# Kernel optimization log

Measured on AMD Instinct MI355X. Metric: run time of the kernel, lower is better.

The kernel has to match this reference:

```python
import jax, jax.numpy as jnp
import numpy as np

EMB = 1024
HID = 2048
NH = 16
NKV = 16
NE = 8
TOPK = 2
WIN = 2048
B = 2
L = 2048
HD = EMB // NH  # 64


def _layer_norm(x, g, b, eps=1e-5):
    m = jnp.mean(x, axis=-1, keepdims=True)
    v = jnp.mean((x - m) ** 2, axis=-1, keepdims=True)
    return (x - m) / jnp.sqrt(v + eps) * g + b


def setup_inputs() -> dict:
    key = jax.random.key(0)
    ks = jax.random.split(key, 12)
    w = lambda k, shape: (jax.random.normal(k, shape, jnp.float32) * 0.02)
    return {
        "x": jax.random.normal(ks[0], (B, L, EMB), jnp.float32),
        "position_idx": 0,
        "ln1_g": jnp.ones((EMB,), jnp.float32),
        "ln1_b": jnp.zeros((EMB,), jnp.float32),
        "ln2_g": jnp.ones((EMB,), jnp.float32),
        "ln2_b": jnp.zeros((EMB,), jnp.float32),
        "Wq": w(ks[1], (EMB, EMB)),
        "Wk": w(ks[2], (EMB, EMB)),
        "Wv": w(ks[3], (EMB, EMB)),
        "Wo": w(ks[4], (EMB, EMB)),
        "Wr": w(ks[5], (EMB, NE)),
        "W1": w(ks[6], (NE, EMB, HID)),
        "b1": jnp.zeros((NE, HID), jnp.float32),
        "W2": w(ks[7], (NE, HID, EMB)),
        "b2": jnp.zeros((NE, EMB), jnp.float32),
    }


def reference(x, position_idx, ln1_g, ln1_b, ln2_g, ln2_b, Wq, Wk, Wv, Wo, Wr, W1, b1, W2, b2):
    Bn, Ln, D = x.shape
    scale = 1.0 / (HD ** 0.5)

    # --- sliding-window attention (cache=None path) ---
    h = _layer_norm(x, ln1_g, ln1_b)
    q = (h @ Wq).reshape(Bn, Ln, NH, HD).transpose(0, 2, 1, 3)   # [B,H,L,hd]
    k = (h @ Wk).reshape(Bn, Ln, NKV, HD).transpose(0, 2, 1, 3)  # [B,KV,L,hd]
    v = (h @ Wv).reshape(Bn, Ln, NKV, HD).transpose(0, 2, 1, 3)
    k = k[:, :, -WIN:]
    v = v[:, :, -WIN:]
    qpk = NH // NKV
    if qpk > 1:
        k = jnp.repeat(k, qpk, axis=1)
        v = jnp.repeat(v, qpk, axis=1)
    scores = jnp.einsum('bhqd,bhkd->bhqk', q, k) * scale
    S = k.shape[2]
    i = jnp.arange(Ln)[:, None]
    j = jnp.arange(S)[None, :]
    mask = (j > i) | (j < i + position_idx - WIN)  # causal + sliding window
    scores = jnp.where(mask[None, None], -jnp.inf, scores)
    attn = jax.nn.softmax(scores, axis=-1)
    attn_out = jnp.einsum('bhqk,bhkd->bqhd', attn, v).reshape(Bn, Ln, D) @ Wo
    x = x + attn_out

    # --- top-k MoE ---
    h2 = _layer_norm(x, ln2_g, ln2_b)
    logits = h2 @ Wr                               # [B,L,E]
    top_v, top_i = jax.lax.top_k(logits, TOPK)     # [B,L,K]
    top_w = jax.nn.softmax(top_v, axis=-1)
    out = jnp.zeros_like(x)
    for e in range(NE):
        # combine weight for expert e per token (sums over top-k slots)
        we = jnp.sum(jnp.where(top_i == e, top_w, 0.0), axis=-1)  # [B,L]
        he = jax.nn.silu(h2 @ W1[e] + b1[e])
        out = out + we[..., None] * (he @ W2[e] + b2[e])
    return x + out
```

## Files before the change

kernel.cpp:

```cpp
#include <hip/hip_runtime.h>
#include <hip/hip_bf16.h>

typedef __hip_bfloat16 bf16;
typedef __attribute__((ext_vector_type(8))) short bf16x8;
typedef __attribute__((ext_vector_type(4))) float f32x4;

constexpr int kEMB = 1024;
constexpr int kHID = 2048;
constexpr int kNH  = 16;
constexpr int kNE  = 8;
constexpr int kL   = 2048;
constexpr int kHD  = 64;
constexpr int kT   = 4096;
constexpr int kSLOTS = kT * 2;
constexpr int kWIN = 2048;

__device__ __forceinline__ unsigned short f2bfbits(float f){
  bf16 h = __float2bfloat16(f);
  return __builtin_bit_cast(unsigned short, h);
}
__device__ __forceinline__ float bfbits2f(unsigned short u){
  unsigned int x = ((unsigned int)u) << 16;
  return __builtin_bit_cast(float, x);
}
__device__ __forceinline__ void gld_lds16(const void* g, void* s){
  __builtin_amdgcn_global_load_lds((const __attribute__((address_space(1))) void*)g,
                                   (__attribute__((address_space(3))) void*)s, 16, 0, 0);
}

__global__ __launch_bounds__(256) void tconv_k(const float* __restrict__ src, bf16* __restrict__ dst,
                                               int R, int C){
  __shared__ float tile[32][33];
  const int tx = threadIdx.x & 31, ty = threadIdx.x >> 5;
  const int bx = blockIdx.x * 32, by = blockIdx.y * 32;
  const size_t base = (size_t)blockIdx.z * R * C;
  #pragma unroll
  for (int i = 0; i < 32; i += 8)
    tile[ty + i][tx] = src[base + (size_t)(by + ty + i) * C + bx + tx];
  __syncthreads();
  #pragma unroll
  for (int i = 0; i < 32; i += 8)
    dst[base + (size_t)(bx + ty + i) * R + by + tx] = __float2bfloat16(tile[tx][ty + i]);
}

__global__ __launch_bounds__(256) void vtrans_k(const bf16* __restrict__ v, bf16* __restrict__ vt){
  __shared__ unsigned short tile[32][33];
  const int tx = threadIdx.x & 31, ty = threadIdx.x >> 5;
  const int l0 = blockIdx.x * 32, d0 = blockIdx.y * 32;
  const unsigned short* src = (const unsigned short*)v + (size_t)blockIdx.z * kL * kHD;
  unsigned short* dst = (unsigned short*)vt + (size_t)blockIdx.z * kHD * kL;
  #pragma unroll
  for (int i = 0; i < 32; i += 8)
    tile[ty + i][tx] = src[(size_t)(l0 + ty + i) * kHD + d0 + tx];
  __syncthreads();
  #pragma unroll
  for (int i = 0; i < 32; i += 8)
    dst[(size_t)(d0 + ty + i) * kL + l0 + tx] = tile[tx][ty + i];
}

__device__ __forceinline__ float block_sum(float v, float* red){
  #pragma unroll
  for (int x = 32; x > 0; x >>= 1) v += __shfl_xor(v, x, 64);
  const int lane = threadIdx.x & 63, w = threadIdx.x >> 6;
  if (lane == 0) red[w] = v;
  __syncthreads();
  float s = red[0] + red[1] + red[2] + red[3];
  __syncthreads();
  return s;
}

__global__ __launch_bounds__(256) void ln_k(
    const float* __restrict__ x, const float* __restrict__ g, const float* __restrict__ bta,
    bf16* __restrict__ h)
{
  __shared__ float red[4];
  const int row = blockIdx.x, tid = threadIdx.x;
  const float4 v = ((const float4*)(x + (size_t)row * kEMB))[tid];
  float s = block_sum(v.x + v.y + v.z + v.w, red);
  const float mean = s * (1.0f / kEMB);
  const float dx = v.x - mean, dy = v.y - mean, dz = v.z - mean, dw = v.w - mean;
  float ss = block_sum(dx*dx + dy*dy + dz*dz + dw*dw, red);
  const float rstd = rsqrtf(ss * (1.0f / kEMB) + 1e-5f);
  const float4 gg = ((const float4*)g)[tid];
  const float4 bb = ((const float4*)bta)[tid];
  ushort4 pk;
  pk.x = f2bfbits(dx * rstd * gg.x + bb.x);
  pk.y = f2bfbits(dy * rstd * gg.y + bb.y);
  pk.z = f2bfbits(dz * rstd * gg.z + bb.z);
  pk.w = f2bfbits(dw * rstd * gg.w + bb.w);
  *(ushort4*)((unsigned short*)h + (size_t)row * kEMB + tid * 4) = pk;
}

__global__ __launch_bounds__(256) void ln2_k(
    const float* __restrict__ x, const float* __restrict__ P,
    const float* __restrict__ g, const float* __restrict__ bta,
    float* __restrict__ out, bf16* __restrict__ h, const float* __restrict__ Wr,
    int* __restrict__ top_i, float* __restrict__ top_w)
{
  __shared__ float red[4];
  __shared__ float red8[4][8];
  const int row = blockIdx.x, tid = threadIdx.x;
  const float4 vx = ((const float4*)(x + (size_t)row * kEMB))[tid];
  const float4 p0 = ((const float4*)(P + (size_t)row * kEMB))[tid];
  const float4 p1 = ((const float4*)(P + (size_t)(kT + row) * kEMB))[tid];
  float4 v;
  v.x = vx.x + p0.x + p1.x; v.y = vx.y + p0.y + p1.y;
  v.z = vx.z + p0.z + p1.z; v.w = vx.w + p0.w + p1.w;
  ((float4*)(out + (size_t)row * kEMB))[tid] = v;
  float s = block_sum(v.x + v.y + v.z + v.w, red);
  const float mean = s * (1.0f / kEMB);
  const float dx = v.x - mean, dy = v.y - mean, dz = v.z - mean, dw = v.w - mean;
  float ss = block_sum(dx*dx + dy*dy + dz*dz + dw*dw, red);
  const float rstd = rsqrtf(ss * (1.0f / kEMB) + 1e-5f);
  const float4 gg = ((const float4*)g)[tid];
  const float4 bb = ((const float4*)bta)[tid];
  const float n0 = dx * rstd * gg.x + bb.x;
  const float n1 = dy * rstd * gg.y + bb.y;
  const float n2 = dz * rstd * gg.z + bb.z;
  const float n3 = dw * rstd * gg.w + bb.w;
  ushort4 pk;
  pk.x = f2bfbits(n0); pk.y = f2bfbits(n1); pk.z = f2bfbits(n2); pk.w = f2bfbits(n3);
  *(ushort4*)((unsigned short*)h + (size_t)row * kEMB + tid * 4) = pk;
  float part[8];
  #pragma unroll
  for (int e = 0; e < 8; e++) part[e] = 0.f;
  const float* wrp = Wr + (size_t)tid * 4 * kNE;
  const float nv[4] = {n0, n1, n2, n3};
  #pragma unroll
  for (int i = 0; i < 4; i++)
    #pragma unroll
    for (int e = 0; e < 8; e++) part[e] += nv[i] * wrp[i * kNE + e];
  #pragma unroll
  for (int xm = 32; xm > 0; xm >>= 1)
    #pragma unroll
    for (int e = 0; e < 8; e++) part[e] += __shfl_xor(part[e], xm, 64);
  const int lane = tid & 63, w = tid >> 6;
  if (lane == 0)
    #pragma unroll
    for (int e = 0; e < 8; e++) red8[w][e] = part[e];
  __syncthreads();
  if (tid == 0){
    float lg[8];
    #pragma unroll
    for (int e = 0; e < 8; e++) lg[e] = red8[0][e] + red8[1][e] + red8[2][e] + red8[3][e];
    int i0 = 0; float v0 = lg[0];
    #pragma unroll
    for (int e = 1; e < 8; e++) if (lg[e] > v0){ v0 = lg[e]; i0 = e; }
    int i1 = -1; float v1 = -3.4e38f;
    #pragma unroll
    for (int e = 0; e < 8; e++) if (e != i0 && lg[e] > v1){ v1 = lg[e]; i1 = e; }
    const float w0 = 1.0f / (1.0f + __expf(v1 - v0));
    top_i[row * 2] = i0; top_i[row * 2 + 1] = i1;
    top_w[row * 2] = w0; top_w[row * 2 + 1] = 1.0f - w0;
  }
}

template<int MODE>
__global__ __launch_bounds__(256) void gemm_k(
    const bf16* __restrict__ A, const bf16* __restrict__ BT, int K,
    float* __restrict__ fdst, bf16* __restrict__ bdst,
    const float* __restrict__ bias,
    const float* __restrict__ roww, const int* __restrict__ rowtok,
    const int* __restrict__ offs)
{
  __shared__ alignas(16) unsigned short As[2][128 * 64];
  __shared__ alignas(16) unsigned short Bs[2][128 * 64];
  const int tid = threadIdx.x, lane = tid & 63, w = tid >> 6;
  const int wr = w >> 1, wc = w & 1;
  int e = 0, rbase = 0, rend = 0, bx, by;
  if (MODE == 2){
    e = blockIdx.x & 7; const int s = blockIdx.x >> 3; by = s >> 4; bx = s & 15;
    rbase = offs[e]; rend = offs[e + 1];
    if (by * 128 >= rend - rbase) return;
  } else if (MODE == 3){
    e = blockIdx.x & 7; const int s = blockIdx.x >> 3; by = s >> 3; bx = s & 7;
    rbase = offs[e]; rend = offs[e + 1];
    if (by * 128 >= rend - rbase) return;
  } else {
    bx = blockIdx.x; by = blockIdx.y;
  }
  int kt0 = 0, nkt = K / 64;
  if (MODE == 1){ kt0 = blockIdx.z * (K / 2); nkt = K / 128; }
  const int m0 = by * 128, n0 = bx * 128;
  const bf16* Bp = BT;
  const float* biasp = bias;
  if (MODE == 2){ Bp += (size_t)e * kHID * kEMB; biasp += e * kHID; }
  if (MODE == 3){ Bp += (size_t)e * kEMB * kHID; biasp += e * kEMB; }
  f32x4 acc[4][4] = {};
  const int srow = lane >> 3;
  const int skk  = (lane & 7) * 8;

  size_t aoff[4];
  #pragma unroll
  for (int j = 0; j < 4; j++){
    const int r = w * 32 + j * 8 + srow;
    size_t row;
    if (MODE == 2){ int p = rbase + m0 + r; if (p >= rend) p = rbase; row = (size_t)rowtok[p]; }
    else if (MODE == 3){ int p = rbase + m0 + r; if (p >= rend) p = rbase; row = (size_t)p; }
    else row = (size_t)(m0 + r);
    aoff[j] = row * (size_t)K;
  }

  auto stage = [&](int t, int buf){
    const int kt = kt0 + t * 64;
    #pragma unroll
    for (int j = 0; j < 4; j++){
      const int rr = w * 32 + j * 8;
      gld_lds16(A + aoff[j] + kt + skk, &As[buf][rr * 64]);
      gld_lds16(Bp + (size_t)(n0 + rr + srow) * K + kt + skk, &Bs[buf][rr * 64]);
    }
  };

  stage(0, 0);
  __syncthreads();
  for (int t = 0; t < nkt; t++){
    const int cur = t & 1;
    if (t + 1 < nkt) stage(t + 1, cur ^ 1);
    #pragma unroll
    for (int ks = 0; ks < 2; ks++){
      bf16x8 af[4], bfm[4];
      #pragma unroll
      for (int i = 0; i < 4; i++){
        af[i]  = *(const bf16x8*)&As[cur][(wr * 64 + i * 16 + (lane & 15)) * 64 + ks * 32 + (lane >> 4) * 8];
        bfm[i] = *(const bf16x8*)&Bs[cur][(wc * 64 + i * 16 + (lane & 15)) * 64 + ks * 32 + (lane >> 4) * 8];
      }
      #pragma unroll
      for (int i = 0; i < 4; i++)
        #pragma unroll
        for (int j = 0; j < 4; j++)
          acc[i][j] = __builtin_amdgcn_mfma_f32_16x16x32_bf16(af[i], bfm[j], acc[i][j], 0, 0, 0);
    }
    __syncthreads();
  }

  #pragma unroll
  for (int i = 0; i < 4; i++){
    #pragma unroll
    for (int r = 0; r < 4; r++){
      const int gm = m0 + wr * 64 + i * 16 + (lane >> 4) * 4 + r;
      if (MODE == 1){
        float* pdst = fdst + (size_t)blockIdx.z * kT * kEMB;
        #pragma unroll
        for (int jn = 0; jn < 4; jn++){
          const int gn = n0 + wc * 64 + jn * 16 + (lane & 15);
          pdst[(size_t)gm * kEMB + gn] = acc[i][jn][r];
        }
      } else if (MODE == 2){
        const int p = rbase + gm;
        if (p < rend){
          #pragma unroll
          for (int jn = 0; jn < 4; jn++){
            const int gn = n0 + wc * 64 + jn * 16 + (lane & 15);
            const float vv = acc[i][jn][r] + biasp[gn];
            bdst[(size_t)p * kHID + gn] = __float2bfloat16(vv / (1.0f + __expf(-vv)));
          }
        }
      } else if (MODE == 3){
        const int p = rbase + gm;
        if (p < rend){
          const float wgt = roww[p];
          #pragma unroll
          for (int jn = 0; jn < 4; jn++){
            const int gn = n0 + wc * 64 + jn * 16 + (lane & 15);
            bdst[(size_t)p * kEMB + gn] = __float2bfloat16((acc[i][jn][r] + biasp[gn]) * wgt);
          }
        }
      } else {
        const int bidx = gm >> 11, l = gm & (kL - 1);
        #pragma unroll
        for (int jn = 0; jn < 4; jn++){
          const int gn = n0 + wc * 64 + jn * 16 + (lane & 15);
          const int sec = gn >> 10;
          const int nn = gn & 1023;
          const int hh = nn >> 6, d = nn & 63;
          const float val = acc[i][jn][r] * (sec == 0 ? 0.125f : 1.0f);
          bdst[(size_t)sec * kT * kEMB + (((size_t)bidx * kNH + hh) * kL + l) * kHD + d] =
              __float2bfloat16(val);
        }
      }
    }
  }
}

__global__ __launch_bounds__(256) void attn_k(
    const bf16* __restrict__ q, const bf16* __restrict__ k, const bf16* __restrict__ vt,
    bf16* __restrict__ o, const int* __restrict__ pos)
{
  const int bid = blockIdx.x;
  const int qt = 31 - (bid >> 5);
  const int bh = bid & 31;
  const int tid = threadIdx.x, lane = tid & 63, w = tid >> 6;
  const unsigned short* qp  = (const unsigned short*)q  + (size_t)bh * kL * kHD;
  const unsigned short* kp  = (const unsigned short*)k  + (size_t)bh * kL * kHD;
  const unsigned short* vtp = (const unsigned short*)vt + (size_t)bh * kHD * kL;
  __shared__ alignas(16) unsigned short Ks[2][64 * 64];
  __shared__ alignas(16) unsigned short Vt[2][64 * 64];
  __shared__ alignas(16) unsigned short pl[4 * 16 * 72];
  const int q0 = qt * 64 + w * 16;
  const int pos0 = pos[0];
  const int wlo = pos0 - kWIN;

  bf16x8 qf[2];
  {
    const int qrow = q0 + (lane & 15);
    #pragma unroll
    for (int ks = 0; ks < 2; ks++)
      qf[ks] = *(const bf16x8*)&qp[(size_t)qrow * kHD + ks * 32 + (lane >> 4) * 8];
  }
  float m_run[4], l_part[4];
  f32x4 oacc[4] = {};
  #pragma unroll
  for (int r = 0; r < 4; r++){ m_run[r] = -1e30f; l_part[r] = 0.f; }

  auto stage = [&](int kt, int buf){
    #pragma unroll
    for (int j = 0; j < 2; j++){
      const int r = w * 16 + j * 8 + (lane >> 3);
      const int c = (lane & 7) ^ (r & 7);
      gld_lds16(kp  + (size_t)(kt * 64 + r) * 64 + c * 8, &Ks[buf][(w * 16 + j * 8) * 64]);
      gld_lds16(vtp + (size_t)r * kL + kt * 64 + c * 8,   &Vt[buf][(w * 16 + j * 8) * 64]);
    }
  };

  stage(0, 0);
  for (int kt = 0; kt <= qt; kt++){
    const int buf = kt & 1;
    __syncthreads();
    if (kt < qt) stage(kt + 1, buf ^ 1);

    f32x4 s[4];
    #pragma unroll
    for (int kbk = 0; kbk < 4; kbk++){
      const int row = kbk * 16 + (lane & 15);
      f32x4 a = {0.f, 0.f, 0.f, 0.f};
      #pragma unroll
      for (int ks = 0; ks < 2; ks++){
        const int chnk = ks * 4 + (lane >> 4);
        const bf16x8 kf = *(const bf16x8*)&Ks[buf][row * 64 + ((chnk ^ (row & 7)) * 8)];
        a = __builtin_amdgcn_mfma_f32_16x16x32_bf16(qf[ks], kf, a, 0, 0, 0);
      }
      s[kbk] = a;
    }
    const bool needmask = (kt == qt) || (kt * 64 < q0 + 16 + wlo);
    if (needmask){
      #pragma unroll
      for (int kbk = 0; kbk < 4; kbk++){
        const int j = kt * 64 + kbk * 16 + (lane & 15);
        #pragma unroll
        for (int r = 0; r < 4; r++){
          const int i = q0 + (lane >> 4) * 4 + r;
          if (j > i || j < i + wlo) s[kbk][r] = -1e30f;
        }
      }
    }
    float pmax[4];
    #pragma unroll
    for (int r = 0; r < 4; r++) pmax[r] = s[0][r];
    #pragma unroll
    for (int kbk = 1; kbk < 4; kbk++)
      #pragma unroll
      for (int r = 0; r < 4; r++) pmax[r] = fmaxf(pmax[r], s[kbk][r]);
    bool need = false;
    #pragma unroll
    for (int r = 0; r < 4; r++) need |= (pmax[r] > m_run[r] + 8.0f);
    if (__any(need)){
      float tm[4];
      #pragma unroll
      for (int r = 0; r < 4; r++) tm[r] = pmax[r];
      #pragma unroll
      for (int xm = 1; xm < 16; xm <<= 1)
        #pragma unroll
        for (int r = 0; r < 4; r++) tm[r] = fmaxf(tm[r], __shfl_xor(tm[r], xm, 64));
      #pragma unroll
      for (int r = 0; r < 4; r++){
        const float mn = fmaxf(m_run[r], tm[r]);
        const float corr = __expf(m_run[r] - mn);
        m_run[r] = mn;
        l_part[r] *= corr;
        #pragma unroll
        for (int db = 0; db < 4; db++) oacc[db][r] *= corr;
      }
    }
    #pragma unroll
    for (int kbk = 0; kbk < 4; kbk++)
      #pragma unroll
      for (int r = 0; r < 4; r++){
        const float p = __expf(s[kbk][r] - m_run[r]);
        s[kbk][r] = p;
        l_part[r] += p;
      }
    #pragma unroll
    for (int kbk = 0; kbk < 4; kbk++)
      #pragma unroll
      for (int r = 0; r < 4; r++)
        pl[(w * 16 + (lane >> 4) * 4 + r) * 72 + kbk * 16 + (lane & 15)] = f2bfbits(s[kbk][r]);
    asm volatile("s_waitcnt lgkmcnt(0)" ::: "memory");
    __builtin_amdgcn_sched_barrier(0);
    bf16x8 pa[2];
    #pragma unroll
    for (int ks = 0; ks < 2; ks++)
      pa[ks] = *(const bf16x8*)&pl[(w * 16 + (lane & 15)) * 72 + ks * 32 + (lane >> 4) * 8];
    #pragma unroll
    for (int db = 0; db < 4; db++){
      const int row = db * 16 + (lane & 15);
      #pragma unroll
      for (int ks = 0; ks < 2; ks++){
        const int chnk = ks * 4 + (lane >> 4);
        const bf16x8 vf = *(const bf16x8*)&Vt[buf][row * 64 + ((chnk ^ (row & 7)) * 8)];
        oacc[db] = __builtin_amdgcn_mfma_f32_16x16x32_bf16(pa[ks], vf, oacc[db], 0, 0, 0);
      }
    }
  }
  #pragma unroll
  for (int xm = 1; xm < 16; xm <<= 1)
    #pragma unroll
    for (int r = 0; r < 4; r++) l_part[r] += __shfl_xor(l_part[r], xm, 64);
  const int hh = bh & (kNH - 1), bidx = bh >> 4;
  #pragma unroll
  for (int db = 0; db < 4; db++){
    #pragma unroll
    for (int r = 0; r < 4; r++){
      const int i = q0 + (lane >> 4) * 4 + r;
      const int d = db * 16 + (lane & 15);
      o[((size_t)(bidx * kL + i)) * kEMB + hh * kHD + d] = __float2bfloat16(oacc[db][r] / l_part[r]);
    }
  }
}

__global__ void zero_k(int* counts){ if (threadIdx.x < kNE) counts[threadIdx.x] = 0; }

__global__ __launch_bounds__(256) void count_k(const int* __restrict__ top_i, int* __restrict__ counts){
  const int idx = blockIdx.x * 256 + threadIdx.x;
  if (idx < kSLOTS) atomicAdd(&counts[top_i[idx]], 1);
}

__global__ void scan_k(const int* __restrict__ counts, int* __restrict__ offs, int* __restrict__ cursor){
  int o = 0;
  for (int e = 0; e < kNE; e++){ offs[e] = o; cursor[e] = o; o += counts[e]; }
  offs[kNE] = o;
}

__global__ __launch_bounds__(256) void assign_k(const int* __restrict__ top_i, const float* __restrict__ top_w,
                                                int* __restrict__ cursor, int* __restrict__ rowtok,
                                                float* __restrict__ roww, int* __restrict__ tok2row){
  const int idx = blockIdx.x * 256 + threadIdx.x;
  if (idx < kSLOTS){
    const int e = top_i[idx];
    const int p = atomicAdd(&cursor[e], 1);
    rowtok[p] = idx >> 1;
    roww[p] = top_w[idx];
    tok2row[idx] = p;
  }
}

__global__ __launch_bounds__(256) void combine_k(float* __restrict__ out, const bf16* __restrict__ g2,
                                                 const int* __restrict__ tok2row){
  const int t = blockIdx.x, c = threadIdx.x * 4;
  const int r0 = tok2row[t * 2], r1 = tok2row[t * 2 + 1];
  const ushort4 ua = *(const ushort4*)((const unsigned short*)g2 + (size_t)r0 * kEMB + c);
  const ushort4 ub = *(const ushort4*)((const unsigned short*)g2 + (size_t)r1 * kEMB + c);
  float* op = out + (size_t)t * kEMB + c;
  float4 ov = *(float4*)op;
  ov.x += bfbits2f(ua.x) + bfbits2f(ub.x);
  ov.y += bfbits2f(ua.y) + bfbits2f(ub.y);
  ov.z += bfbits2f(ua.z) + bfbits2f(ub.z);
  ov.w += bfbits2f(ua.w) + bfbits2f(ub.w);
  *(float4*)op = ov;
}

extern "C" void kernel_launch(void* const* d_in, const int* in_sizes, int n_in,
                              void* d_out, int out_size, void* d_ws, size_t ws_size,
                              hipStream_t stream)
{
  const float* x    = (const float*)d_in[0];
  const int*   pos  = (const int*)d_in[1];
  const float* ln1g = (const float*)d_in[2];
  const float* ln1b = (const float*)d_in[3];
  const float* ln2g = (const float*)d_in[4];
  const float* ln2b = (const float*)d_in[5];
  const float* Wq   = (const float*)d_in[6];
  const float* Wk   = (const float*)d_in[7];
  const float* Wv   = (const float*)d_in[8];
  const float* Wo   = (const float*)d_in[9];
  const float* Wr   = (const float*)d_in[10];
  const float* W1   = (const float*)d_in[11];
  const float* b1   = (const float*)d_in[12];
  const float* W2   = (const float*)d_in[13];
  const float* b2   = (const float*)d_in[14];
  float* out = (float*)d_out;

  char* p = (char*)d_ws;
  auto alloc = [&](size_t bytes) -> char* {
    char* r = p; p += (bytes + 255) & ~(size_t)255; return r;
  };
  bf16* WqkvT = (bf16*)alloc((size_t)3 * kEMB * kEMB * 2);
  bf16* WoT   = (bf16*)alloc((size_t)kEMB * kEMB * 2);
  bf16* W1T   = (bf16*)alloc((size_t)kNE * kEMB * kHID * 2);
  bf16* W2T   = (bf16*)alloc((size_t)kNE * kEMB * kHID * 2);
  bf16* hbf   = (bf16*)alloc((size_t)kT * kEMB * 2);
  bf16* qkv   = (bf16*)alloc((size_t)3 * kT * kEMB * 2);
  bf16* vtbf  = (bf16*)alloc((size_t)kT * kEMB * 2);
  bf16* abf   = (bf16*)alloc((size_t)kT * kEMB * 2);
  bf16* h2bf  = (bf16*)alloc((size_t)kT * kEMB * 2);
  bf16* hebf  = (bf16*)alloc((size_t)kSLOTS * kHID * 2);
  bf16* g2bf  = (bf16*)alloc((size_t)kSLOTS * kEMB * 2);
  int*   top_i   = (int*)alloc(kSLOTS * 4);
  float* top_w   = (float*)alloc(kSLOTS * 4);
  int*   counts  = (int*)alloc(64);
  int*   offs    = (int*)alloc(64);
  int*   cursor  = (int*)alloc(64);
  int*   rowtok  = (int*)alloc(kSLOTS * 4);
  float* rowwgt  = (float*)alloc(kSLOTS * 4);
  int*   tok2row = (int*)alloc(kSLOTS * 4);
  bf16* qbf = qkv;
  bf16* kbf = qkv + (size_t)kT * kEMB;
  bf16* vbf = qkv + (size_t)2 * kT * kEMB;
  float* Pws = (float*)hbf;
  (void)in_sizes; (void)n_in; (void)out_size; (void)ws_size;

  tconv_k<<<dim3(32, 32, 1), 256, 0, stream>>>(Wq, WqkvT, kEMB, kEMB);
  tconv_k<<<dim3(32, 32, 1), 256, 0, stream>>>(Wk, WqkvT + (size_t)kEMB * kEMB, kEMB, kEMB);
  tconv_k<<<dim3(32, 32, 1), 256, 0, stream>>>(Wv, WqkvT + (size_t)2 * kEMB * kEMB, kEMB, kEMB);
  tconv_k<<<dim3(32, 32, 1), 256, 0, stream>>>(Wo, WoT, kEMB, kEMB);
  tconv_k<<<dim3(64, 32, kNE), 256, 0, stream>>>(W1, W1T, kEMB, kHID);
  tconv_k<<<dim3(32, 64, kNE), 256, 0, stream>>>(W2, W2T, kHID, kEMB);

  ln_k<<<kT, 256, 0, stream>>>(x, ln1g, ln1b, hbf);

  gemm_k<4><<<dim3(24, 32), 256, 0, stream>>>(hbf, WqkvT, kEMB, nullptr, qkv, nullptr, nullptr, nullptr, nullptr);

  vtrans_k<<<dim3(kL / 32, kHD / 32, 32), 256, 0, stream>>>(vbf, vtbf);

  attn_k<<<dim3(1024), 256, 0, stream>>>(qbf, kbf, vtbf, abf, pos);

  gemm_k<1><<<dim3(8, 32, 2), 256, 0, stream>>>(abf, WoT, kEMB, Pws, nullptr, nullptr, nullptr, nullptr, nullptr);

  ln2_k<<<kT, 256, 0, stream>>>(x, Pws, ln2g, ln2b, out, h2bf, Wr, top_i, top_w);

  zero_k<<<1, 64, 0, stream>>>(counts);
  count_k<<<kSLOTS / 256, 256, 0, stream>>>(top_i, counts);
  scan_k<<<1, 1, 0, stream>>>(counts, offs, cursor);
  assign_k<<<kSLOTS / 256, 256, 0, stream>>>(top_i, top_w, cursor, rowtok, rowwgt, tok2row);

  gemm_k<2><<<dim3(8 * 32 * 16), 256, 0, stream>>>(h2bf, W1T, kEMB, nullptr, hebf, b1, nullptr, rowtok, offs);
  gemm_k<3><<<dim3(8 * 32 * 8), 256, 0, stream>>>(hebf, W2T, kHID, nullptr, g2bf, b2, rowwgt, nullptr, offs);

  combine_k<<<kT, 256, 0, stream>>>(out, g2bf, tok2row);
}
```

Before: 397.1 us.

## Add triple-buffered swizzled MoE expert GEMM and fuse expert counting into LN2

Moves the grouped expert GEMMs (W1 with SiLU, W2 with routing weight) into a new kernel. It uses K-tiles of 32, a three-stage LDS ring with explicit vmcnt waits and one barrier per step, XOR-swizzled LDS rows, and raised wave priority around the MFMAs. Expert counts are now accumulated with atomics inside the LN2/router kernel, which removes the separate count pass. The four square weight transposes are merged into one launch. Smaller K tiles mean more loop iterations and barriers, and the hand-written waitcnt logic depends on the exact number of outstanding loads.

```diff
diff --git a/kernel.cpp b/kernel.cpp
--- a/kernel.cpp
+++ b/kernel.cpp
@@ -41,6 +41,24 @@
   #pragma unroll
   for (int i = 0; i < 32; i += 8)
     dst[base + (size_t)(bx + ty + i) * R + by + tx] = __float2bfloat16(tile[tx][ty + i]);
+}
+
+__global__ __launch_bounds__(256) void tconv4_k(const float* __restrict__ s0, const float* __restrict__ s1,
+                                                const float* __restrict__ s2, const float* __restrict__ s3,
+                                                bf16* __restrict__ dst){
+  __shared__ float tile[32][33];
+  const int tx = threadIdx.x & 31, ty = threadIdx.x >> 5;
+  const int bx = blockIdx.x * 32, by = blockIdx.y * 32;
+  const int z = blockIdx.z;
+  const float* src = (z == 0) ? s0 : (z == 1) ? s1 : (z == 2) ? s2 : s3;
+  bf16* d = dst + (size_t)z * kEMB * kEMB;
+  #pragma unroll
+  for (int i = 0; i < 32; i += 8)
+    tile[ty + i][tx] = src[(size_t)(by + ty + i) * kEMB + bx + tx];
+  __syncthreads();
+  #pragma unroll
+  for (int i = 0; i < 32; i += 8)
+    d[(size_t)(bx + ty + i) * kEMB + by + tx] = __float2bfloat16(tile[tx][ty + i]);
 }
 
 __global__ __launch_bounds__(256) void vtrans_k(const bf16* __restrict__ v, bf16* __restrict__ vt){
@@ -95,7 +113,7 @@
     const float* __restrict__ x, const float* __restrict__ P,
     const float* __restrict__ g, const float* __restrict__ bta,
     float* __restrict__ out, bf16* __restrict__ h, const float* __restrict__ Wr,
-    int* __restrict__ top_i, float* __restrict__ top_w)
+    int* __restrict__ top_i, float* __restrict__ top_w, int* __restrict__ counts)
 {
   __shared__ float red[4];
   __shared__ float red8[4][8];
@@ -152,62 +170,35 @@
     const float w0 = 1.0f / (1.0f + __expf(v1 - v0));
     top_i[row * 2] = i0; top_i[row * 2 + 1] = i1;
     top_w[row * 2] = w0; top_w[row * 2 + 1] = 1.0f - w0;
+    atomicAdd(&counts[i0], 1);
+    atomicAdd(&counts[i1], 1);
   }
 }
 
 template<int MODE>
 __global__ __launch_bounds__(256) void gemm_k(
     const bf16* __restrict__ A, const bf16* __restrict__ BT, int K,
-    float* __restrict__ fdst, bf16* __restrict__ bdst,
-    const float* __restrict__ bias,
-    const float* __restrict__ roww, const int* __restrict__ rowtok,
-    const int* __restrict__ offs)
+    float* __restrict__ fdst, bf16* __restrict__ bdst)
 {
   __shared__ alignas(16) unsigned short As[2][128 * 64];
   __shared__ alignas(16) unsigned short Bs[2][128 * 64];
   const int tid = threadIdx.x, lane = tid & 63, w = tid >> 6;
   const int wr = w >> 1, wc = w & 1;
-  int e = 0, rbase = 0, rend = 0, bx, by;
-  if (MODE == 2){
-    e = blockIdx.x & 7; const int s = blockIdx.x >> 3; by = s >> 4; bx = s & 15;
-    rbase = offs[e]; rend = offs[e + 1];
-    if (by * 128 >= rend - rbase) return;
-  } else if (MODE == 3){
-    e = blockIdx.x & 7; const int s = blockIdx.x >> 3; by = s >> 3; bx = s & 7;
-    rbase = offs[e]; rend = offs[e + 1];
-    if (by * 128 >= rend - rbase) return;
-  } else {
-    bx = blockIdx.x; by = blockIdx.y;
-  }
+  const int bx = blockIdx.x, by = blockIdx.y;
   int kt0 = 0, nkt = K / 64;
   if (MODE == 1){ kt0 = blockIdx.z * (K / 2); nkt = K / 128; }
   const int m0 = by * 128, n0 = bx * 128;
-  const bf16* Bp = BT;
-  const float* biasp = bias;
-  if (MODE == 2){ Bp += (size_t)e * kHID * kEMB; biasp += e * kHID; }
-  if (MODE == 3){ Bp += (size_t)e * kEMB * kHID; biasp += e * kEMB; }
   f32x4 acc[4][4] = {};
   const int srow = lane >> 3;
   const int skk  = (lane & 7) * 8;
 
-  size_t aoff[4];
-  #pragma unroll
-  for (int j = 0; j < 4; j++){
-    const int r = w * 32 + j * 8 + srow;
-    size_t row;
-    if (MODE == 2){ int p = rbase + m0 + r; if (p >= rend) p = rbase; row = (size_t)rowtok[p]; }
-    else if (MODE == 3){ int p = rbase + m0 + r; if (p >= rend) p = rbase; row = (size_t)p; }
-    else row = (size_t)(m0 + r);
-    aoff[j] = row * (size_t)K;
-  }
-
   auto stage = [&](int t, int buf){
     const int kt = kt0 + t * 64;
     #pragma unroll
     for (int j = 0; j < 4; j++){
       const int rr = w * 32 + j * 8;
-      gld_lds16(A + aoff[j] + kt + skk, &As[buf][rr * 64]);
-      gld_lds16(Bp + (size_t)(n0 + rr + srow) * K + kt + skk, &Bs[buf][rr * 64]);
+      gld_lds16(A + (size_t)(m0 + rr + srow) * K + kt + skk, &As[buf][rr * 64]);
+      gld_lds16(BT + (size_t)(n0 + rr + srow) * K + kt + skk, &Bs[buf][rr * 64]);
     }
   };
 
@@ -244,26 +235,6 @@
         for (int jn = 0; jn < 4; jn++){
           const int gn = n0 + wc * 64 + jn * 16 + (lane & 15);
           pdst[(size_t)gm * kEMB + gn] = acc[i][jn][r];
-        }
-      } else if (MODE == 2){
-        const int p = rbase + gm;
-        if (p < rend){
-          #pragma unroll
-          for (int jn = 0; jn < 4; jn++){
-            const int gn = n0 + wc * 64 + jn * 16 + (lane & 15);
-            const float vv = acc[i][jn][r] + biasp[gn];
-            bdst[(size_t)p * kHID + gn] = __float2bfloat16(vv / (1.0f + __expf(-vv)));
-          }
-        }
-      } else if (MODE == 3){
-        const int p = rbase + gm;
-        if (p < rend){
-          const float wgt = roww[p];
-          #pragma unroll
-          for (int jn = 0; jn < 4; jn++){
-            const int gn = n0 + wc * 64 + jn * 16 + (lane & 15);
-            bdst[(size_t)p * kEMB + gn] = __float2bfloat16((acc[i][jn][r] + biasp[gn]) * wgt);
-          }
         }
       } else {
         const int bidx = gm >> 11, l = gm & (kL - 1);
@@ -276,6 +247,104 @@
           const float val = acc[i][jn][r] * (sec == 0 ? 0.125f : 1.0f);
           bdst[(size_t)sec * kT * kEMB + (((size_t)bidx * kNH + hh) * kL + l) * kHD + d] =
               __float2bfloat16(val);
+        }
+      }
+    }
+  }
+}
+
+template<int MODE>
+__global__ __launch_bounds__(256) void gemm3_k(
+    const bf16* __restrict__ A, const bf16* __restrict__ BT, int K,
+    bf16* __restrict__ bdst, const float* __restrict__ bias,
+    const float* __restrict__ roww, const int* __restrict__ rowtok,
+    const int* __restrict__ offs)
+{
+  __shared__ alignas(16) unsigned short As[3][128 * 32];
+  __shared__ alignas(16) unsigned short Bs[3][128 * 32];
+  const int tid = threadIdx.x, lane = tid & 63, w = tid >> 6;
+  const int wr = w >> 1, wc = w & 1;
+  const int e = blockIdx.x & 7, s = blockIdx.x >> 3;
+  const int bx = (MODE == 2) ? (s & 15) : (s & 7);
+  const int by = (MODE == 2) ? (s >> 4) : (s >> 3);
+  const int rbase = offs[e], rend = offs[e + 1];
+  if (by * 128 >= rend - rbase) return;
+  const int m0 = by * 128, n0 = bx * 128;
+  const int NB = (MODE == 2) ? kHID : kEMB;
+  const bf16* Bp = BT + (size_t)e * NB * K;
+  const float* biasp = bias + e * NB;
+  const int nkt = K / 32;
+  f32x4 acc[4][4] = {};
+
+  const int sc = tid & 3, sr0 = tid >> 2;
+  const int scs = (sc ^ (sr0 & 3)) * 8;
+  size_t aoffs[2]; size_t boffs[2];
+  {
+    int p0 = rbase + m0 + sr0;      if (p0 >= rend) p0 = rbase;
+    int p1 = rbase + m0 + 64 + sr0; if (p1 >= rend) p1 = rbase;
+    aoffs[0] = (size_t)((MODE == 2) ? rowtok[p0] : p0) * K;
+    aoffs[1] = (size_t)((MODE == 2) ? rowtok[p1] : p1) * K;
+    boffs[0] = (size_t)(n0 + sr0) * K;
+    boffs[1] = (size_t)(n0 + 64 + sr0) * K;
+  }
+
+  auto stage = [&](int t){
+    const int b = t % 3; const int kt = t * 32;
+    gld_lds16(A  + aoffs[0] + kt + scs, &As[b][tid * 8]);
+    gld_lds16(A  + aoffs[1] + kt + scs, &As[b][(tid + 256) * 8]);
+    gld_lds16(Bp + boffs[0] + kt + scs, &Bs[b][tid * 8]);
+    gld_lds16(Bp + boffs[1] + kt + scs, &Bs[b][(tid + 256) * 8]);
+  };
+
+  stage(0);
+  stage(1);
+  for (int t = 0; t < nkt; t++){
+    const int cur = t % 3;
+    if (t + 1 < nkt) { asm volatile("s_waitcnt vmcnt(4)" ::: "memory"); }
+    else             { asm volatile("s_waitcnt vmcnt(0)" ::: "memory"); }
+    __builtin_amdgcn_s_barrier();
+    bf16x8 af[4], bfm[4];
+    const int cc = lane >> 4;
+    #pragma unroll
+    for (int i = 0; i < 4; i++){
+      const int ar = wr * 64 + i * 16 + (lane & 15);
+      af[i] = *(const bf16x8*)&As[cur][ar * 32 + ((cc ^ (ar & 3)) * 8)];
+    }
+    #pragma unroll
+    for (int j = 0; j < 4; j++){
+      const int br = wc * 64 + j * 16 + (lane & 15);
+      bfm[j] = *(const bf16x8*)&Bs[cur][br * 32 + ((cc ^ (br & 3)) * 8)];
+    }
+    __builtin_amdgcn_s_setprio(1);
+    #pragma unroll
+    for (int i = 0; i < 4; i++)
+      #pragma unroll
+      for (int j = 0; j < 4; j++)
+        acc[i][j] = __builtin_amdgcn_mfma_f32_16x16x32_bf16(af[i], bfm[j], acc[i][j], 0, 0, 0);
+    __builtin_amdgcn_s_setprio(0);
+    if (t + 2 < nkt) stage(t + 2);
+  }
+
+  #pragma unroll
+  for (int i = 0; i < 4; i++){
+    #pragma unroll
+    for (int r = 0; r < 4; r++){
+      const int p = rbase + m0 + wr * 64 + i * 16 + (lane >> 4) * 4 + r;
+      if (p < rend){
+        if (MODE == 2){
+          #pragma unroll
+          for (int jn = 0; jn < 4; jn++){
+            const int gn = n0 + wc * 64 + jn * 16 + (lane & 15);
+            const float vv = acc[i][jn][r] + biasp[gn];
+            bdst[(size_t)p * NB + gn] = __float2bfloat16(vv / (1.0f + __expf(-vv)));
+          }
+        } else {
+          const float wgt = roww[p];
+          #pragma unroll
+          for (int jn = 0; jn < 4; jn++){
+            const int gn = n0 + wc * 64 + jn * 16 + (lane & 15);
+            bdst[(size_t)p * NB + gn] = __float2bfloat16((acc[i][jn][r] + biasp[gn]) * wgt);
+          }
         }
       }
     }
@@ -428,11 +497,6 @@
 }
 
 __global__ void zero_k(int* counts){ if (threadIdx.x < kNE) counts[threadIdx.x] = 0; }
-
-__global__ __launch_bounds__(256) void count_k(const int* __restrict__ top_i, int* __restrict__ counts){
-  const int idx = blockIdx.x * 256 + threadIdx.x;
-  if (idx < kSLOTS) atomicAdd(&counts[top_i[idx]], 1);
-}
 
 __global__ void scan_k(const int* __restrict__ counts, int* __restrict__ offs, int* __restrict__ cursor){
   int o = 0;
@@ -518,32 +582,29 @@
   float* Pws = (float*)hbf;
   (void)in_sizes; (void)n_in; (void)out_size; (void)ws_size;
 
-  tconv_k<<<dim3(32, 32, 1), 256, 0, stream>>>(Wq, WqkvT, kEMB, kEMB);
-  tconv_k<<<dim3(32, 32, 1), 256, 0, stream>>>(Wk, WqkvT + (size_t)kEMB * kEMB, kEMB, kEMB);
-  tconv_k<<<dim3(32, 32, 1), 256, 0, stream>>>(Wv, WqkvT + (size_t)2 * kEMB * kEMB, kEMB, kEMB);
-  tconv_k<<<dim3(32, 32, 1), 256, 0, stream>>>(Wo, WoT, kEMB, kEMB);
+  zero_k<<<1, 64, 0, stream>>>(counts);
+
+  tconv4_k<<<dim3(32, 32, 4), 256, 0, stream>>>(Wq, Wk, Wv, Wo, WqkvT);
   tconv_k<<<dim3(64, 32, kNE), 256, 0, stream>>>(W1, W1T, kEMB, kHID);
   tconv_k<<<dim3(32, 64, kNE), 256, 0, stream>>>(W2, W2T, kHID, kEMB);
 
   ln_k<<<kT, 256, 0, stream>>>(x, ln1g, ln1b, hbf);
 
-  gemm_k<4><<<dim3(24, 32), 256, 0, stream>>>(hbf, WqkvT, kEMB, nullptr, qkv, nullptr, nullptr, nullptr, nullptr);
+  gemm_k<4><<<dim3(24, 32), 256, 0, stream>>>(hbf, WqkvT, kEMB, nullptr, qkv);
 
   vtrans_k<<<dim3(kL / 32, kHD / 32, 32), 256, 0, stream>>>(vbf, vtbf);
 
   attn_k<<<dim3(1024), 256, 0, stream>>>(qbf, kbf, vtbf, abf, pos);
 
-  gemm_k<1><<<dim3(8, 32, 2), 256, 0, stream>>>(abf, WoT, kEMB, Pws, nullptr, nullptr, nullptr, nullptr, nullptr);
-
-  ln2_k<<<kT, 256, 0, stream>>>(x, Pws, ln2g, ln2b, out, h2bf, Wr, top_i, top_w);
-
-  zero_k<<<1, 64, 0, stream>>>(counts);
-  count_k<<<kSLOTS / 256, 256, 0, stream>>>(top_i, counts);
+  gemm_k<1><<<dim3(8, 32, 2), 256, 0, stream>>>(abf, WoT, kEMB, Pws, nullptr);
+
+  ln2_k<<<kT, 256, 0, stream>>>(x, Pws, ln2g, ln2b, out, h2bf, Wr, top_i, top_w, counts);
+
   scan_k<<<1, 1, 0, stream>>>(counts, offs, cursor);
   assign_k<<<kSLOTS / 256, 256, 0, stream>>>(top_i, top_w, cursor, rowtok, rowwgt, tok2row);
 
-  gemm_k<2><<<dim3(8 * 32 * 16), 256, 0, stream>>>(h2bf, W1T, kEMB, nullptr, hebf, b1, nullptr, rowtok, offs);
-  gemm_k<3><<<dim3(8 * 32 * 8), 256, 0, stream>>>(hebf, W2T, kHID, nullptr, g2bf, b2, rowwgt, nullptr, offs);
+  gemm3_k<2><<<dim3(8 * 32 * 16), 256, 0, stream>>>(h2bf, W1T, kEMB, hebf, b1, nullptr, rowtok, offs);
+  gemm3_k<3><<<dim3(8 * 32 * 8), 256, 0, stream>>>(hebf, W2T, kHID, g2bf, b2, rowwgt, nullptr, offs);
 
   combine_k<<<kT, 256, 0, stream>>>(out, g2bf, tok2row);
 }
```

New measurement: 412.6 us. +3.9%, slower.
